# Kernel optimization log

Hardware: AMD Instinct MI355X
Metric: run time of the kernel (lower is better)

The kernel has to match this reference:

```python
import jax, jax.numpy as jnp
import numpy as np

NEG = -1e10  # the original uses -10000000000.0
B, T, L = 64, 512, 64
START, END = 0, L - 1


def setup_inputs() -> dict:
    key = jax.random.key(0)
    k_em, k_tr, k_len = jax.random.split(key, 3)
    emission_scores = jax.random.normal(k_em, (B, T, L), dtype=jnp.float32)
    # transition initialized as in __init__: randn with start column / end row masked
    transition = jax.random.normal(k_tr, (L, L), dtype=jnp.float32)
    transition = transition.at[:, START].set(NEG)
    transition = transition.at[END, :].set(NEG)
    sent_lens = jax.random.randint(k_len, (B,), T // 2, T + 1, dtype=jnp.int32)
    return {"emission_scores": emission_scores, "transition": transition,
            "sent_lens": sent_lens}


def reference(emission_scores, transition, sent_lens):
    # --- calculate_all_scores ---
    em = emission_scores.at[:, :, START].set(NEG).at[:, :, END].set(NEG)
    # scores[b,t,y_prev,y_t] = transition[y_prev,y_t] + emission[b,t,y_t]
    scores = transition[None, None, :, :] + em[:, :, None, :]  # [B,T,L,L]
    scores = scores.at[:, 1:, START, :].set(NEG)

    # --- forward_score: sequential DP via scan ---
    alpha0 = scores[:, 0, START, :]  # [B,L]

    def step(alpha_prev, s_t):  # s_t: [B,L,L]
        alpha_t = jax.nn.logsumexp(alpha_prev[:, :, None] + s_t, axis=1)
        return alpha_t, alpha_t

    _, alphas_rest = jax.lax.scan(step, alpha0, jnp.moveaxis(scores[:, 1:], 1, 0))
    alpha = jnp.concatenate([alpha0[:, None, :], jnp.moveaxis(alphas_rest, 0, 1)],
                            axis=1)  # [B,T,L]

    idx = (sent_lens - 1).astype(jnp.int32)[:, None, None]  # [B,1,1]
    last_alpha = jnp.take_along_axis(alpha, idx, axis=1)[:, 0, :]  # [B,L]
    last_alpha = last_alpha + transition[:, END][None, :]
    log_Z = jax.nn.logsumexp(last_alpha, axis=1)  # [B]
    return alpha, log_Z
```

## Files before the change

### kernel.cpp

```cpp
#include <hip/hip_runtime.h>

#define NEGV -10000000000.0f
constexpr int Bn = 64, Tn = 512, Ln = 64;
constexpr int CK = 32;
constexpr int NC = 16;
constexpr int QP = 64;

typedef float f32x16 __attribute__((ext_vector_type(16)));
typedef __bf16 bf16x8 __attribute__((ext_vector_type(8)));
typedef unsigned int u32;
typedef unsigned short u16;
typedef unsigned int u32x2 __attribute__((ext_vector_type(2)));

__device__ inline float waveMaxF(float v) {
#pragma unroll
    for (int off = 32; off > 0; off >>= 1)
        v = fmaxf(v, __shfl_xor(v, off, 64));
    return v;
}
__device__ inline u32 packbf(float a, float b) {
    u32 ua = __float_as_uint(a) + 0x8000u;
    u32 ub = __float_as_uint(b) + 0x8000u;
    return (ua >> 16) | (ub & 0xffff0000u);
}
__device__ inline u32 cvtpk(float a, float b) {
    u32 r;
    asm("v_cvt_pk_bf16_f32 %0, %1, %2" : "=v"(r) : "v"(a), "v"(b));
    return r;
}
__device__ inline void swap32(u32& x, u32& y) {
    u32x2 r = __builtin_amdgcn_permlane32_swap(x, y, false, false);
    x = r.x;
    y = r.y;
}
__device__ inline float lo16f(u32 d) { return __uint_as_float(d << 16); }
__device__ inline float hi16f(u32 d) { return __uint_as_float(d & 0xffff0000u); }

template <bool FIRST>
__device__ void chunk_scan(const float* __restrict__ emb,
                           float* __restrict__ outb, float* uLDS,
                           const float* Ecol, float entry, int t0, int j, int len,
                           float trSj, float* aLastOut, float* aFinalOut) {
    const bool edge = (j == 0) || (j == Ln - 1);
    float emq[4];
#pragma unroll
    for (int tt = 0; tt < 4; ++tt) {
        float v = emb[(t0 + tt) * Ln + j];
        emq[tt] = edge ? NEGV : v;
    }
    float aPrev, mPrev, u;
    int tauStart;
    if (FIRST) {
        float a0 = trSj + emq[0];
        outb[t0 * Ln + j] = a0;
        aPrev = a0;
        mPrev = __shfl(a0, 1, 64);
        u = __expf(a0 - mPrev);
        tauStart = 1;
    } else {
        aPrev = entry;
        mPrev = __shfl(entry, 1, 64);
        u = __expf(entry - mPrev);
        tauStart = 0;
    }
    float aLast = *aLastOut;
#pragma unroll 4
    for (int tau = tauStart; tau < CK; ++tau) {
        const int t = t0 + tau;
        uLDS[j] = u;
        const float em_t = emq[tau & 3];
        const int tp = tau + 4;
        if (tp < CK) {
            float v = emb[(t0 + tp) * Ln + j];
            emq[tp & 3] = edge ? NEGV : v;
        }
        float mNext = __shfl(aPrev, 1, 64);
        float cf = __expf(em_t + (mPrev - mNext));
        float acc0 = 0.f, acc1 = 0.f, acc2 = 0.f, acc3 = 0.f;
        const float4* u4 = reinterpret_cast<const float4*>(uLDS);
#pragma unroll
        for (int i4 = 0; i4 < 16; ++i4) {
            float4 uv = u4[i4];
            acc0 = fmaf(uv.x, Ecol[4 * i4 + 0], acc0);
            acc1 = fmaf(uv.y, Ecol[4 * i4 + 1], acc1);
            acc2 = fmaf(uv.z, Ecol[4 * i4 + 2], acc2);
            acc3 = fmaf(uv.w, Ecol[4 * i4 + 3], acc3);
        }
        float S = (acc0 + acc1) + (acc2 + acc3);
        float lg = __logf(S);
        lg = (S > 0.f) ? lg : NEGV;
        float a_t = em_t + (mPrev + lg);
        outb[t * Ln + j] = a_t;
        if (t == len - 1) aLast = a_t;
        u = S * cf;
        aPrev = a_t;
        mPrev = mNext;
    }
    *aLastOut = aLast;
    *aFinalOut = aPrev;
}

__global__ __launch_bounds__(128) void crf_passA(const float* __restrict__ em,
                                                 const float* __restrict__ tr,
                                                 float* __restrict__ out,
                                                 float* __restrict__ wsE,
                                                 float* __restrict__ wsS) {
    const int b = blockIdx.x & 63;
    const int cix = blockIdx.x >> 6;
    const int J = threadIdx.x >> 6;
    const int L = threadIdx.x & 63;
    __shared__ alignas(16) float gtab[CK * 64];
    __shared__ alignas(16) u16 Qlds[64 * QP];
    __shared__ alignas(16) float uLDS[64];
    __shared__ float sLDS[2];
    __shared__ float sigLDS[2];

    if (cix == 0) {
        if (J == 1) return;
        float Ecol[Ln];
#pragma unroll
        for (int i = 0; i < Ln; ++i) Ecol[i] = __expf(tr[i * Ln + L]);
        const float trSj = tr[L];
        const float* emb = em + (size_t)b * Tn * Ln;
        float* outb = out + (size_t)b * Tn * Ln;
        float dummyLast = 0.f, aFinal;
        chunk_scan<true>(emb, outb, uLDS, Ecol, 0.f, 0, L,  -1, trSj, &dummyLast, &aFinal);
        wsE[b * 1024 + 1 * 64 + L] = aFinal;
        return;
    }

    const int t0 = CK * cix;
    const int c31 = L & 31;
    const int h = L >> 5;

    {
        float orig[16], sv[16];
        const int tb = t0 + 16 * J;
#pragma unroll
        for (int r = 0; r < 16; ++r) {
            float v = em[((size_t)b * Tn + (tb + r)) * Ln + L];
            if (L == 0 || L == Ln - 1) v = NEGV;
            orig[r] = v;
            sv[r] = v;
        }
#pragma unroll
        for (int off = 32; off > 0; off >>= 1) {
#pragma unroll
            for (int r = 0; r < 16; ++r)
                sv[r] = fmaxf(sv[r], __shfl_xor(sv[r], off, 64));
        }
        float ssum = 0.f;
#pragma unroll
        for (int r = 0; r < 16; ++r) {
            gtab[(16 * J + r) * 64 + L] = __expf(orig[r] - sv[r]);
            ssum += sv[r];
        }
        if (L == 0) sLDS[J] = ssum;
    }
    __syncthreads();
    const float sSum = sLDS[0] + sLDS[1];

    uint4 Ap[2][4];
#pragma unroll
    for (int I = 0; I < 2; ++I)
#pragma unroll
        for (int kc = 0; kc < 4; ++kc) {
            float e[8];
#pragma unroll
            for (int q = 0; q < 8; ++q) {
                int k = 16 * kc + 8 * h + q;
                e[q] = __expf(tr[k * Ln + 32 * I + c31]);
            }
            Ap[I][kc] = make_uint4(packbf(e[0], e[1]), packbf(e[2], e[3]),
                                   packbf(e[4], e[5]), packbf(e[6], e[7]));
        }

    const int n = 32 * J + c31;
    uint4 Bp[4];
    {
        const float* trn = tr + n * Ln;
#pragma unroll
        for (int kc = 0; kc < 4; ++kc) {
            float v[8];
#pragma unroll
            for (int q = 0; q < 8; ++q) {
                const int k = 16 * kc + 8 * h + q;
                v[q] = __expf(trn[k]) * gtab[k];
            }
            Bp[kc] = make_uint4(cvtpk(v[0], v[1]), cvtpk(v[2], v[3]),
                                cvtpk(v[4], v[5]), cvtpk(v[6], v[7]));
        }
    }

    float sig_w = 0.f;
    float wm = 1.0f;
    const f32x16 Z = (f32x16)(0.0f);
    for (int tau = 1; tau < CK; ++tau) {
        f32x16 acc0 = Z, acc1 = Z;
#pragma unroll
        for (int kc = 0; kc < 4; ++kc) {
            acc0 = __builtin_amdgcn_mfma_f32_32x32x16_bf16(
                __builtin_bit_cast(bf16x8, Ap[0][kc]),
                __builtin_bit_cast(bf16x8, Bp[kc]), acc0, 0, 0, 0);
            acc1 = __builtin_amdgcn_mfma_f32_32x32x16_bf16(
                __builtin_bit_cast(bf16x8, Ap[1][kc]),
                __builtin_bit_cast(bf16x8, Bp[kc]), acc1, 0, 0, 0);
        }
        const bool doRescale = ((tau & 3) == 0);
        const bool doMeasure = ((tau & 3) == 2);
        float rr = 1.0f;
        if (doRescale) {
            rr = 1.0f / wm;
            sig_w += __logf(wm);
        }
        float lmax = 0.f;
        const float* gt = gtab + tau * 64;
#pragma unroll
        for (int I = 0; I < 2; ++I) {
            u32 pp[8];
#pragma unroll
            for (int rg = 0; rg < 4; ++rg) {
                const int k0 = 32 * I + 8 * rg + 4 * h;
                float4 G = *(const float4*)&gt[k0];
                float v0 = (I ? acc1 : acc0)[4 * rg + 0] * (G.x * rr);
                float v1 = (I ? acc1 : acc0)[4 * rg + 1] * (G.y * rr);
                float v2 = (I ? acc1 : acc0)[4 * rg + 2] * (G.z * rr);
                float v3 = (I ? acc1 : acc0)[4 * rg + 3] * (G.w * rr);
                if (doMeasure) lmax = fmaxf(lmax, fmaxf(fmaxf(v0, v1), fmaxf(v2, v3)));
                pp[2 * rg + 0] = cvtpk(v0, v1);
                pp[2 * rg + 1] = cvtpk(v2, v3);
            }
            swap32(pp[0], pp[2]);
            swap32(pp[1], pp[3]);
            swap32(pp[4], pp[6]);
            swap32(pp[5], pp[7]);
            Bp[2 * I + 0] = make_uint4(pp[0], pp[1], pp[2], pp[3]);
            Bp[2 * I + 1] = make_uint4(pp[4], pp[5], pp[6], pp[7]);
        }
        if (doMeasure) wm = waveMaxF(lmax);
    }

#pragma unroll
    for (int kc = 0; kc < 4; ++kc)
        *(uint4*)&Qlds[n * QP + 16 * kc + 8 * h] = Bp[kc];

    if (L == 0) sigLDS[J] = sSum + sig_w;
    __syncthreads();
    const float sg0 = sigLDS[0], sg1 = sigLDS[1];
    const float smax = fmaxf(sg0, sg1);
    const float fh = __expf((h ? sg1 : sg0) - smax);
    const int r = 32 * J + c31;
    float rv[32];
    float lmaxr = 0.f;
#pragma unroll
    for (int i = 0; i < 32; ++i) {
        float v = __uint_as_float(((u32)Qlds[(32 * h + i) * QP + r]) << 16) * fh;
        rv[i] = v;
        lmaxr = fmaxf(lmaxr, v);
    }
    float rmax = fmaxf(lmaxr, __shfl_xor(lmaxr, 32, 64));
    float inv = (rmax > 0.f) ? 1.0f / rmax : 0.f;
    float sj = (rmax > 0.f) ? smax + __logf(rmax) : 0.f;
    u32* og = (u32*)out + (size_t)b * (Tn * Ln) + (size_t)cix * (CK * Ln) + r * 32 + h * 16;
#pragma unroll
    for (int w8 = 0; w8 < 4; ++w8) {
        uint4 w;
        w.x = packbf(rv[8 * w8 + 0] * inv, rv[8 * w8 + 1] * inv);
        w.y = packbf(rv[8 * w8 + 2] * inv, rv[8 * w8 + 3] * inv);
        w.z = packbf(rv[8 * w8 + 4] * inv, rv[8 * w8 + 5] * inv);
        w.w = packbf(rv[8 * w8 + 6] * inv, rv[8 * w8 + 7] * inv);
        *(uint4*)(og + 4 * w8) = w;
    }
    if (h == 0) wsS[b * 1024 + cix * 64 + r] = sj;
}

__global__ __launch_bounds__(64) void crf_passB(const float* __restrict__ out,
                                                float* __restrict__ wsE,
                                                const float* __restrict__ wsS) {
    const int b = blockIdx.x;
    const int j = threadIdx.x;
    __shared__ alignas(16) float uL[64];
    const u32* Qbase = (const u32*)out + (size_t)b * (Tn * Ln);

    float e = wsE[b * 1024 + 1 * 64 + j];
    uint4 nxt[8];
    float signxt = wsS[b * 1024 + 1 * 64 + j];
#pragma unroll
    for (int r = 0; r < 8; ++r) nxt[r] = *(const uint4*)(Qbase + 1 * (CK * Ln) + j * 32 + 4 * r);

#pragma unroll
    for (int c = 1; c <= 14; ++c) {
        uint4 cur[8];
#pragma unroll
        for (int r = 0; r < 8; ++r) cur[r] = nxt[r];
        float sig = signxt;
        if (c < 14) {
#pragma unroll
            for (int r = 0; r < 8; ++r)
                nxt[r] = *(const uint4*)(Qbase + (size_t)(c + 1) * (CK * Ln) + j * 32 + 4 * r);
            signxt = wsS[b * 1024 + (c + 1) * 64 + j];
        }
        float m = __shfl(e, 1, 64);
        uL[j] = __expf(e - m);
        const float4* u4 = reinterpret_cast<const float4*>(uL);
        float S = 0.f;
#pragma unroll
        for (int i4 = 0; i4 < 16; ++i4) {
            float4 uv = u4[i4];
            u32 d0 = ((const u32*)cur)[2 * i4];
            u32 d1 = ((const u32*)cur)[2 * i4 + 1];
            S = fmaf(uv.x, lo16f(d0), S);
            S = fmaf(uv.y, hi16f(d0), S);
            S = fmaf(uv.z, lo16f(d1), S);
            S = fmaf(uv.w, hi16f(d1), S);
        }
        float a;
        if (S > 0.f) a = m + sig + __logf(S);
        else a = m + NEGV + ((j == 0) ? NEGV : 0.f);
        e = a;
        wsE[b * 1024 + (c + 1) * 64 + j] = e;
    }
}

__global__ __launch_bounds__(64) void crf_passC(const float* __restrict__ em,
                                                const float* __restrict__ tr,
                                                const int* __restrict__ lens,
                                                float* __restrict__ out,
                                                const float* __restrict__ wsE) {
    const int b = blockIdx.x & 63;
    const int cix = 1 + (blockIdx.x >> 6);
    const int j = threadIdx.x;
    __shared__ alignas(16) float uLDS[64];

    float Ecol[Ln];
#pragma unroll
    for (int i = 0; i < Ln; ++i) Ecol[i] = __expf(tr[i * Ln + j]);
    const float trEj = tr[j * Ln + (Ln - 1)];
    const int len = lens[b];
    const float* emb = em + (size_t)b * Tn * Ln;
    float* outb = out + (size_t)b * Tn * Ln;
    const float entry = wsE[b * 1024 + cix * 64 + j];

    float aLast = 0.f, aFinal;
    chunk_scan<false>(emb, outb, uLDS, Ecol, entry, CK * cix, j, len, 0.f, &aLast, &aFinal);

    if (((len - 1) >> 5) == cix) {
        float last = aLast + trEj;
        float m2 = last;
#pragma unroll
        for (int off = 32; off > 0; off >>= 1)
            m2 = fmaxf(m2, __shfl_xor(m2, off, 64));
        float e2 = __expf(last - m2);
#pragma unroll
        for (int off = 32; off > 0; off >>= 1)
            e2 += __shfl_xor(e2, off, 64);
        if (j == 0) out[(size_t)Bn * Tn * Ln + b] = m2 + __logf(e2);
    }
}

__global__ __launch_bounds__(64) void crf_fallback(const float* __restrict__ em,
                                                   const float* __restrict__ tr,
                                                   const int* __restrict__ lens,
                                                   float* __restrict__ out) {
    const int b = blockIdx.x;
    const int j = threadIdx.x;
    __shared__ alignas(16) float uLDS[Ln];
    float E[Ln];
#pragma unroll
    for (int i = 0; i < Ln; ++i) E[i] = __expf(tr[i * Ln + j]);
    const float trSj = tr[j];
    const float trEj = tr[j * Ln + (Ln - 1)];
    const int len = lens[b];
    const bool edge = (j == 0) || (j == Ln - 1);
    const float* emb = em + (size_t)b * Tn * Ln;
    float* outb = out + (size_t)b * Tn * Ln;
    float emq[4];
#pragma unroll
    for (int tt = 0; tt < 4; ++tt) {
        float v = emb[tt * Ln + j];
        emq[tt] = edge ? NEGV : v;
    }
    float a = trSj + emq[0];
    outb[j] = a;
    float aPrev = a, aLast = a;
    float mPrev = __shfl(a, 1, 64);
    float u = __expf(a - mPrev);
#pragma unroll 4
    for (int t = 1; t < Tn; ++t) {
        uLDS[j] = u;
        const float em_t = emq[t & 3];
        const int tp = t + 4;
        if (tp < Tn) {
            float v = emb[tp * Ln + j];
            emq[tp & 3] = edge ? NEGV : v;
        }
        float mNext = __shfl(aPrev, 1, 64);
        float cf = __expf(em_t + (mPrev - mNext));
        float acc0 = 0.f, acc1 = 0.f, acc2 = 0.f, acc3 = 0.f;
        const float4* u4 = reinterpret_cast<const float4*>(uLDS);
#pragma unroll
        for (int i4 = 0; i4 < 16; ++i4) {
            float4 uv = u4[i4];
            acc0 = fmaf(uv.x, E[4 * i4 + 0], acc0);
            acc1 = fmaf(uv.y, E[4 * i4 + 1], acc1);
            acc2 = fmaf(uv.z, E[4 * i4 + 2], acc2);
            acc3 = fmaf(uv.w, E[4 * i4 + 3], acc3);
        }
        float S = (acc0 + acc1) + (acc2 + acc3);
        float lg = __logf(S);
        lg = (S > 0.f) ? lg : NEGV;
        float a_t = em_t + (mPrev + lg);
        outb[t * Ln + j] = a_t;
        if (t == len - 1) aLast = a_t;
        u = S * cf;
        aPrev = a_t;
        mPrev = mNext;
    }
    float last = aLast + trEj;
    float m2 = last;
#pragma unroll
    for (int off = 32; off > 0; off >>= 1)
        m2 = fmaxf(m2, __shfl_xor(m2, off, 64));
    float e2 = __expf(last - m2);
#pragma unroll
    for (int off = 32; off > 0; off >>= 1)
        e2 += __shfl_xor(e2, off, 64);
    if (j == 0) out[(size_t)Bn * Tn * Ln + b] = m2 + __logf(e2);
}

extern "C" void kernel_launch(void* const* d_in, const int* in_sizes, int n_in,
                              void* d_out, int out_size, void* d_ws, size_t ws_size,
                              hipStream_t stream) {
    const float* em = (const float*)d_in[0];
    const float* tr = (const float*)d_in[1];
    const int* lens = (const int*)d_in[2];
    float* out = (float*)d_out;
    const size_t wsNeed = 2u * 64 * 16 * 64 * sizeof(float);
    if (ws_size >= wsNeed) {
        float* wsE = (float*)d_ws;
        float* wsS = wsE + 64 * 16 * 64;
        crf_passA<<<dim3(1024), dim3(128), 0, stream>>>(em, tr, out, wsE, wsS);
        crf_passB<<<dim3(64), dim3(64), 0, stream>>>(out, wsE, wsS);
        crf_passC<<<dim3(960), dim3(64), 0, stream>>>(em, tr, lens, out, wsE);
    } else {
        crf_fallback<<<dim3(Bn), dim3(64), 0, stream>>>(em, tr, lens, out);
    }
}
```

Before: 126.4 us.

## Split per-chunk transfer-matrix product into two half-chunk waves pairs and merge via MFMA

Pass A now uses four waves per block: one pair computes the forward product of the first half of the 32-step chunk, the other pair computes the second half (built from transposed transitions in reverse). The two half-chunk products are then combined with one extra MFMA matrix multiply through swizzled LDS. This halves the serial dependency chain of MFMA steps per chunk. In exchange it adds extra LDS traffic, barriers and a merge step, doubles the threads per block, and may change bf16 rounding behaviour.

```diff
diff --git a/kernel.cpp b/kernel.cpp
--- a/kernel.cpp
+++ b/kernel.cpp
@@ -35,6 +35,39 @@
 }
 __device__ inline float lo16f(u32 d) { return __uint_as_float(d << 16); }
 __device__ inline float hi16f(u32 d) { return __uint_as_float(d & 0xffff0000u); }
+
+__device__ inline void c2b(const f32x16& a0, const f32x16& a1, const float* gt,
+                           float rr, bool useG, bool doMeasure, float& lmax,
+                           uint4* Bp, int h) {
+#pragma unroll
+    for (int I = 0; I < 2; ++I) {
+        u32 pp[8];
+#pragma unroll
+        for (int rg = 0; rg < 4; ++rg) {
+            const int k0 = 32 * I + 8 * rg + 4 * h;
+            float gx, gy, gz, gw;
+            if (useG) {
+                float4 G = *(const float4*)&gt[k0];
+                gx = G.x * rr; gy = G.y * rr; gz = G.z * rr; gw = G.w * rr;
+            } else {
+                gx = gy = gz = gw = rr;
+            }
+            float v0 = (I ? a1 : a0)[4 * rg + 0] * gx;
+            float v1 = (I ? a1 : a0)[4 * rg + 1] * gy;
+            float v2 = (I ? a1 : a0)[4 * rg + 2] * gz;
+            float v3 = (I ? a1 : a0)[4 * rg + 3] * gw;
+            if (doMeasure) lmax = fmaxf(lmax, fmaxf(fmaxf(v0, v1), fmaxf(v2, v3)));
+            pp[2 * rg + 0] = cvtpk(v0, v1);
+            pp[2 * rg + 1] = cvtpk(v2, v3);
+        }
+        swap32(pp[0], pp[2]);
+        swap32(pp[1], pp[3]);
+        swap32(pp[4], pp[6]);
+        swap32(pp[5], pp[7]);
+        Bp[2 * I + 0] = make_uint4(pp[0], pp[1], pp[2], pp[3]);
+        Bp[2 * I + 1] = make_uint4(pp[4], pp[5], pp[6], pp[7]);
+    }
+}
 
 template <bool FIRST>
 __device__ void chunk_scan(const float* __restrict__ emb,
@@ -100,23 +133,25 @@
     *aFinalOut = aPrev;
 }
 
-__global__ __launch_bounds__(128) void crf_passA(const float* __restrict__ em,
-                                                 const float* __restrict__ tr,
-                                                 float* __restrict__ out,
-                                                 float* __restrict__ wsE,
-                                                 float* __restrict__ wsS) {
+__global__ __launch_bounds__(256, 4) void crf_passA(const float* __restrict__ em,
+                                                    const float* __restrict__ tr,
+                                                    float* __restrict__ out,
+                                                    float* __restrict__ wsE,
+                                                    float* __restrict__ wsS) {
     const int b = blockIdx.x & 63;
     const int cix = blockIdx.x >> 6;
     const int J = threadIdx.x >> 6;
     const int L = threadIdx.x & 63;
+    const int J2 = J & 1;
+    const int pair = J >> 1;
     __shared__ alignas(16) float gtab[CK * 64];
     __shared__ alignas(16) u16 Qlds[64 * QP];
     __shared__ alignas(16) float uLDS[64];
-    __shared__ float sLDS[2];
-    __shared__ float sigLDS[2];
+    __shared__ float sLDS[4];
+    __shared__ float sigLDS[4];
 
     if (cix == 0) {
-        if (J == 1) return;
+        if (J != 0) return;
         float Ecol[Ln];
 #pragma unroll
         for (int i = 0; i < Ln; ++i) Ecol[i] = __expf(tr[i * Ln + L]);
@@ -134,10 +169,10 @@
     const int h = L >> 5;
 
     {
-        float orig[16], sv[16];
-        const int tb = t0 + 16 * J;
-#pragma unroll
-        for (int r = 0; r < 16; ++r) {
+        float orig[8], sv[8];
+        const int tb = t0 + 8 * J;
+#pragma unroll
+        for (int r = 0; r < 8; ++r) {
             float v = em[((size_t)b * Tn + (tb + r)) * Ln + L];
             if (L == 0 || L == Ln - 1) v = NEGV;
             orig[r] = v;
@@ -146,19 +181,19 @@
 #pragma unroll
         for (int off = 32; off > 0; off >>= 1) {
 #pragma unroll
-            for (int r = 0; r < 16; ++r)
+            for (int r = 0; r < 8; ++r)
                 sv[r] = fmaxf(sv[r], __shfl_xor(sv[r], off, 64));
         }
         float ssum = 0.f;
 #pragma unroll
-        for (int r = 0; r < 16; ++r) {
-            gtab[(16 * J + r) * 64 + L] = __expf(orig[r] - sv[r]);
+        for (int r = 0; r < 8; ++r) {
+            gtab[(8 * J + r) * 64 + L] = __expf(orig[r] - sv[r]);
             ssum += sv[r];
         }
         if (L == 0) sLDS[J] = ssum;
     }
     __syncthreads();
-    const float sSum = sLDS[0] + sLDS[1];
+    const float sSeg = sLDS[2 * pair] + sLDS[2 * pair + 1];
 
     uint4 Ap[2][4];
 #pragma unroll
@@ -169,15 +204,16 @@
 #pragma unroll
             for (int q = 0; q < 8; ++q) {
                 int k = 16 * kc + 8 * h + q;
-                e[q] = __expf(tr[k * Ln + 32 * I + c31]);
+                int m = 32 * I + c31;
+                e[q] = __expf(pair ? tr[m * Ln + k] : tr[k * Ln + m]);
             }
             Ap[I][kc] = make_uint4(packbf(e[0], e[1]), packbf(e[2], e[3]),
                                    packbf(e[4], e[5]), packbf(e[6], e[7]));
         }
 
-    const int n = 32 * J + c31;
+    const int n = 32 * J2 + c31;
     uint4 Bp[4];
-    {
+    if (pair == 0) {
         const float* trn = tr + n * Ln;
 #pragma unroll
         for (int kc = 0; kc < 4; ++kc) {
@@ -190,12 +226,25 @@
             Bp[kc] = make_uint4(cvtpk(v[0], v[1]), cvtpk(v[2], v[3]),
                                 cvtpk(v[4], v[5]), cvtpk(v[6], v[7]));
         }
+    } else {
+        const float gn = gtab[31 * 64 + n];
+#pragma unroll
+        for (int kc = 0; kc < 4; ++kc) {
+            float v[8];
+#pragma unroll
+            for (int q = 0; q < 8; ++q) {
+                const int k = 16 * kc + 8 * h + q;
+                v[q] = __expf(tr[k * Ln + n]) * gtab[30 * 64 + k] * gn;
+            }
+            Bp[kc] = make_uint4(cvtpk(v[0], v[1]), cvtpk(v[2], v[3]),
+                                cvtpk(v[4], v[5]), cvtpk(v[6], v[7]));
+        }
     }
 
     float sig_w = 0.f;
     float wm = 1.0f;
     const f32x16 Z = (f32x16)(0.0f);
-    for (int tau = 1; tau < CK; ++tau) {
+    for (int lt = 1; lt <= 15; ++lt) {
         f32x16 acc0 = Z, acc1 = Z;
 #pragma unroll
         for (int kc = 0; kc < 4; ++kc) {
@@ -206,46 +255,77 @@
                 __builtin_bit_cast(bf16x8, Ap[1][kc]),
                 __builtin_bit_cast(bf16x8, Bp[kc]), acc1, 0, 0, 0);
         }
-        const bool doRescale = ((tau & 3) == 0);
-        const bool doMeasure = ((tau & 3) == 2);
+        const bool doRescale = ((lt & 3) == 0);
+        const bool doMeasure = ((lt & 3) == 2);
         float rr = 1.0f;
         if (doRescale) {
             rr = 1.0f / wm;
             sig_w += __logf(wm);
         }
+        const int grow = pair ? (30 - lt) : lt;
+        const bool useG = !(pair && lt == 15);
         float lmax = 0.f;
-        const float* gt = gtab + tau * 64;
-#pragma unroll
-        for (int I = 0; I < 2; ++I) {
-            u32 pp[8];
-#pragma unroll
-            for (int rg = 0; rg < 4; ++rg) {
-                const int k0 = 32 * I + 8 * rg + 4 * h;
-                float4 G = *(const float4*)&gt[k0];
-                float v0 = (I ? acc1 : acc0)[4 * rg + 0] * (G.x * rr);
-                float v1 = (I ? acc1 : acc0)[4 * rg + 1] * (G.y * rr);
-                float v2 = (I ? acc1 : acc0)[4 * rg + 2] * (G.z * rr);
-                float v3 = (I ? acc1 : acc0)[4 * rg + 3] * (G.w * rr);
-                if (doMeasure) lmax = fmaxf(lmax, fmaxf(fmaxf(v0, v1), fmaxf(v2, v3)));
-                pp[2 * rg + 0] = cvtpk(v0, v1);
-                pp[2 * rg + 1] = cvtpk(v2, v3);
+        c2b(acc0, acc1, gtab + grow * 64, rr, useG, doMeasure, lmax, Bp, h);
+        if (doMeasure) wm = waveMaxF(lmax);
+    }
+
+    if (L == 0) sigLDS[J] = sSeg + sig_w;
+    __syncthreads();
+    const float smax1 = fmaxf(sigLDS[2], sigLDS[3]);
+
+    if (pair == 1) {
+        const float fh1 = __expf(sigLDS[J] - smax1);
+        const u32 swz = (u32)(n & 7) << 4;
+        char* base = (char*)Qlds;
+#pragma unroll
+        for (int kc = 0; kc < 4; ++kc) {
+            uint4 w = Bp[kc];
+            float s0 = lo16f(w.x) * fh1, s1 = hi16f(w.x) * fh1;
+            float s2 = lo16f(w.y) * fh1, s3 = hi16f(w.y) * fh1;
+            float s4 = lo16f(w.z) * fh1, s5 = hi16f(w.z) * fh1;
+            float s6 = lo16f(w.w) * fh1, s7 = hi16f(w.w) * fh1;
+            uint4 o = make_uint4(cvtpk(s0, s1), cvtpk(s2, s3), cvtpk(s4, s5), cvtpk(s6, s7));
+            *(uint4*)(base + (((u32)(n * 128 + 32 * kc + 16 * h)) ^ swz)) = o;
+        }
+    }
+    __syncthreads();
+
+    uint4 BpZ[4];
+    if (pair == 0) {
+        uint4 Ah[2][4];
+        const char* cbase = (const char*)Qlds;
+#pragma unroll
+        for (int I = 0; I < 2; ++I)
+#pragma unroll
+            for (int kc = 0; kc < 4; ++kc) {
+                const int m = 32 * I + c31;
+                Ah[I][kc] = *(const uint4*)(cbase +
+                    (((u32)(m * 128 + 32 * kc + 16 * h)) ^ ((u32)(m & 7) << 4)));
             }
-            swap32(pp[0], pp[2]);
-            swap32(pp[1], pp[3]);
-            swap32(pp[4], pp[6]);
-            swap32(pp[5], pp[7]);
-            Bp[2 * I + 0] = make_uint4(pp[0], pp[1], pp[2], pp[3]);
-            Bp[2 * I + 1] = make_uint4(pp[4], pp[5], pp[6], pp[7]);
-        }
-        if (doMeasure) wm = waveMaxF(lmax);
-    }
-
-#pragma unroll
-    for (int kc = 0; kc < 4; ++kc)
-        *(uint4*)&Qlds[n * QP + 16 * kc + 8 * h] = Bp[kc];
-
-    if (L == 0) sigLDS[J] = sSum + sig_w;
+        f32x16 acc0 = Z, acc1 = Z;
+#pragma unroll
+        for (int kc = 0; kc < 4; ++kc) {
+            acc0 = __builtin_amdgcn_mfma_f32_32x32x16_bf16(
+                __builtin_bit_cast(bf16x8, Ah[0][kc]),
+                __builtin_bit_cast(bf16x8, Bp[kc]), acc0, 0, 0, 0);
+            acc1 = __builtin_amdgcn_mfma_f32_32x32x16_bf16(
+                __builtin_bit_cast(bf16x8, Ah[1][kc]),
+                __builtin_bit_cast(bf16x8, Bp[kc]), acc1, 0, 0, 0);
+        }
+        float dummy = 0.f;
+        c2b(acc0, acc1, nullptr, 1.0f, false, false, dummy, BpZ, h);
+    }
     __syncthreads();
+
+    if (pair == 0) {
+#pragma unroll
+        for (int kc = 0; kc < 4; ++kc)
+            *(uint4*)&Qlds[n * QP + 16 * kc + 8 * h] = BpZ[kc];
+        if (L == 0) sigLDS[J] += smax1;
+    }
+    __syncthreads();
+    if (pair == 1) return;
+
     const float sg0 = sigLDS[0], sg1 = sigLDS[1];
     const float smax = fmaxf(sg0, sg1);
     const float fh = __expf((h ? sg1 : sg0) - smax);
@@ -439,7 +519,7 @@
     if (ws_size >= wsNeed) {
         float* wsE = (float*)d_ws;
         float* wsS = wsE + 64 * 16 * 64;
-        crf_passA<<<dim3(1024), dim3(128), 0, stream>>>(em, tr, out, wsE, wsS);
+        crf_passA<<<dim3(1024), dim3(256), 0, stream>>>(em, tr, out, wsE, wsS);
         crf_passB<<<dim3(64), dim3(64), 0, stream>>>(out, wsE, wsS);
         crf_passC<<<dim3(960), dim3(64), 0, stream>>>(em, tr, lens, out, wsE);
     } else {
```

New measurement: 138.0 us. +9.2%, slower.

## Halve chunk length, precompute exp(transition) tables, stage chunk matrices in workspace

Applied to the files above, without the earlier changes.

Chunk length drops from 32 to 16 steps, doubling the chunks per sequence so the per-chunk matrix scan and the final per-chunk rescan (passC) are shorter and more parallel. The serial combine pass (passB) now runs 30 steps instead of 14. A new pre-kernel computes exp(transition) once, in fp32 and as a transposed bf16 table, so passA and passC load it instead of recomputing exp per block. Chunk transfer matrices now go to a dedicated workspace buffer instead of being parked in the output, at the cost of an extra launch and more workspace traffic.

```diff
diff --git a/kernel.cpp b/kernel.cpp
--- a/kernel.cpp
+++ b/kernel.cpp
@@ -2,9 +2,10 @@
 
 #define NEGV -10000000000.0f
 constexpr int Bn = 64, Tn = 512, Ln = 64;
-constexpr int CK = 32;
-constexpr int NC = 16;
+constexpr int CK = 16;
+constexpr int NC = 32;
 constexpr int QP = 64;
+constexpr int WS = 2048;
 
 typedef float f32x16 __attribute__((ext_vector_type(16)));
 typedef __bf16 bf16x8 __attribute__((ext_vector_type(8)));
@@ -35,6 +36,42 @@
 }
 __device__ inline float lo16f(u32 d) { return __uint_as_float(d << 16); }
 __device__ inline float hi16f(u32 d) { return __uint_as_float(d & 0xffff0000u); }
+
+__device__ inline void c2b(const f32x16& a0, const f32x16& a1, const float* gt,
+                           float rr, bool doMeasure, float& lmax, uint4* Bp, int h) {
+#pragma unroll
+    for (int I = 0; I < 2; ++I) {
+        u32 pp[8];
+#pragma unroll
+        for (int rg = 0; rg < 4; ++rg) {
+            const int k0 = 32 * I + 8 * rg + 4 * h;
+            float4 G = *(const float4*)&gt[k0];
+            float v0 = (I ? a1 : a0)[4 * rg + 0] * (G.x * rr);
+            float v1 = (I ? a1 : a0)[4 * rg + 1] * (G.y * rr);
+            float v2 = (I ? a1 : a0)[4 * rg + 2] * (G.z * rr);
+            float v3 = (I ? a1 : a0)[4 * rg + 3] * (G.w * rr);
+            if (doMeasure) lmax = fmaxf(lmax, fmaxf(fmaxf(v0, v1), fmaxf(v2, v3)));
+            pp[2 * rg + 0] = cvtpk(v0, v1);
+            pp[2 * rg + 1] = cvtpk(v2, v3);
+        }
+        swap32(pp[0], pp[2]);
+        swap32(pp[1], pp[3]);
+        swap32(pp[4], pp[6]);
+        swap32(pp[5], pp[7]);
+        Bp[2 * I + 0] = make_uint4(pp[0], pp[1], pp[2], pp[3]);
+        Bp[2 * I + 1] = make_uint4(pp[4], pp[5], pp[6], pp[7]);
+    }
+}
+
+__global__ __launch_bounds__(64) void crf_pre(const float* __restrict__ tr,
+                                              float* __restrict__ tblR,
+                                              u16* __restrict__ tblT) {
+    const int id = blockIdx.x * 64 + threadIdx.x;
+    tblR[id] = __expf(tr[id]);
+    const int m = id >> 6, k = id & 63;
+    float ev = __expf(tr[k * Ln + m]);
+    tblT[id] = (u16)cvtpk(ev, ev);
+}
 
 template <bool FIRST>
 __device__ void chunk_scan(const float* __restrict__ emb,
@@ -102,9 +139,12 @@
 
 __global__ __launch_bounds__(128) void crf_passA(const float* __restrict__ em,
                                                  const float* __restrict__ tr,
+                                                 const float* __restrict__ tblR,
+                                                 const u16* __restrict__ tblT,
                                                  float* __restrict__ out,
                                                  float* __restrict__ wsE,
-                                                 float* __restrict__ wsS) {
+                                                 float* __restrict__ wsS,
+                                                 u32* __restrict__ wsT) {
     const int b = blockIdx.x & 63;
     const int cix = blockIdx.x >> 6;
     const int J = threadIdx.x >> 6;
@@ -119,13 +159,13 @@
         if (J == 1) return;
         float Ecol[Ln];
 #pragma unroll
-        for (int i = 0; i < Ln; ++i) Ecol[i] = __expf(tr[i * Ln + L]);
+        for (int i = 0; i < Ln; ++i) Ecol[i] = tblR[i * Ln + L];
         const float trSj = tr[L];
         const float* emb = em + (size_t)b * Tn * Ln;
         float* outb = out + (size_t)b * Tn * Ln;
         float dummyLast = 0.f, aFinal;
         chunk_scan<true>(emb, outb, uLDS, Ecol, 0.f, 0, L,  -1, trSj, &dummyLast, &aFinal);
-        wsE[b * 1024 + 1 * 64 + L] = aFinal;
+        wsE[b * WS + 1 * 64 + L] = aFinal;
         return;
     }
 
@@ -134,10 +174,10 @@
     const int h = L >> 5;
 
     {
-        float orig[16], sv[16];
-        const int tb = t0 + 16 * J;
-#pragma unroll
-        for (int r = 0; r < 16; ++r) {
+        float orig[8], sv[8];
+        const int tb = t0 + 8 * J;
+#pragma unroll
+        for (int r = 0; r < 8; ++r) {
             float v = em[((size_t)b * Tn + (tb + r)) * Ln + L];
             if (L == 0 || L == Ln - 1) v = NEGV;
             orig[r] = v;
@@ -146,13 +186,13 @@
 #pragma unroll
         for (int off = 32; off > 0; off >>= 1) {
 #pragma unroll
-            for (int r = 0; r < 16; ++r)
+            for (int r = 0; r < 8; ++r)
                 sv[r] = fmaxf(sv[r], __shfl_xor(sv[r], off, 64));
         }
         float ssum = 0.f;
 #pragma unroll
-        for (int r = 0; r < 16; ++r) {
-            gtab[(16 * J + r) * 64 + L] = __expf(orig[r] - sv[r]);
+        for (int r = 0; r < 8; ++r) {
+            gtab[(8 * J + r) * 64 + L] = __expf(orig[r] - sv[r]);
             ssum += sv[r];
         }
         if (L == 0) sLDS[J] = ssum;
@@ -161,34 +201,30 @@
     const float sSum = sLDS[0] + sLDS[1];
 
     uint4 Ap[2][4];
-#pragma unroll
-    for (int I = 0; I < 2; ++I)
-#pragma unroll
-        for (int kc = 0; kc < 4; ++kc) {
-            float e[8];
-#pragma unroll
-            for (int q = 0; q < 8; ++q) {
-                int k = 16 * kc + 8 * h + q;
-                e[q] = __expf(tr[k * Ln + 32 * I + c31]);
-            }
-            Ap[I][kc] = make_uint4(packbf(e[0], e[1]), packbf(e[2], e[3]),
-                                   packbf(e[4], e[5]), packbf(e[6], e[7]));
-        }
+    {
+        const uint4* Af = (const uint4*)tblT;
+#pragma unroll
+        for (int I = 0; I < 2; ++I)
+#pragma unroll
+            for (int kc = 0; kc < 4; ++kc)
+                Ap[I][kc] = Af[(32 * I + c31) * 8 + 2 * kc + h];
+    }
 
     const int n = 32 * J + c31;
     uint4 Bp[4];
     {
-        const float* trn = tr + n * Ln;
+        const float* trn = tblR + n * Ln;
 #pragma unroll
         for (int kc = 0; kc < 4; ++kc) {
-            float v[8];
-#pragma unroll
-            for (int q = 0; q < 8; ++q) {
-                const int k = 16 * kc + 8 * h + q;
-                v[q] = __expf(trn[k]) * gtab[k];
-            }
-            Bp[kc] = make_uint4(cvtpk(v[0], v[1]), cvtpk(v[2], v[3]),
-                                cvtpk(v[4], v[5]), cvtpk(v[6], v[7]));
+            const int k0 = 16 * kc + 8 * h;
+            float4 e0 = *(const float4*)&trn[k0];
+            float4 e1 = *(const float4*)&trn[k0 + 4];
+            float4 g0 = *(const float4*)&gtab[k0];
+            float4 g1 = *(const float4*)&gtab[k0 + 4];
+            Bp[kc] = make_uint4(cvtpk(e0.x * g0.x, e0.y * g0.y),
+                                cvtpk(e0.z * g0.z, e0.w * g0.w),
+                                cvtpk(e1.x * g1.x, e1.y * g1.y),
+                                cvtpk(e1.z * g1.z, e1.w * g1.w));
         }
     }
 
@@ -214,29 +250,7 @@
             sig_w += __logf(wm);
         }
         float lmax = 0.f;
-        const float* gt = gtab + tau * 64;
-#pragma unroll
-        for (int I = 0; I < 2; ++I) {
-            u32 pp[8];
-#pragma unroll
-            for (int rg = 0; rg < 4; ++rg) {
-                const int k0 = 32 * I + 8 * rg + 4 * h;
-                float4 G = *(const float4*)&gt[k0];
-                float v0 = (I ? acc1 : acc0)[4 * rg + 0] * (G.x * rr);
-                float v1 = (I ? acc1 : acc0)[4 * rg + 1] * (G.y * rr);
-                float v2 = (I ? acc1 : acc0)[4 * rg + 2] * (G.z * rr);
-                float v3 = (I ? acc1 : acc0)[4 * rg + 3] * (G.w * rr);
-                if (doMeasure) lmax = fmaxf(lmax, fmaxf(fmaxf(v0, v1), fmaxf(v2, v3)));
-                pp[2 * rg + 0] = cvtpk(v0, v1);
-                pp[2 * rg + 1] = cvtpk(v2, v3);
-            }
-            swap32(pp[0], pp[2]);
-            swap32(pp[1], pp[3]);
-            swap32(pp[4], pp[6]);
-            swap32(pp[5], pp[7]);
-            Bp[2 * I + 0] = make_uint4(pp[0], pp[1], pp[2], pp[3]);
-            Bp[2 * I + 1] = make_uint4(pp[4], pp[5], pp[6], pp[7]);
-        }
+        c2b(acc0, acc1, gtab + tau * 64, rr, doMeasure, lmax, Bp, h);
         if (doMeasure) wm = waveMaxF(lmax);
     }
 
@@ -261,7 +275,7 @@
     float rmax = fmaxf(lmaxr, __shfl_xor(lmaxr, 32, 64));
     float inv = (rmax > 0.f) ? 1.0f / rmax : 0.f;
     float sj = (rmax > 0.f) ? smax + __logf(rmax) : 0.f;
-    u32* og = (u32*)out + (size_t)b * (Tn * Ln) + (size_t)cix * (CK * Ln) + r * 32 + h * 16;
+    u32* og = wsT + (size_t)(b * NC + cix) * 2048 + r * 32 + h * 16;
 #pragma unroll
     for (int w8 = 0; w8 < 4; ++w8) {
         uint4 w;
@@ -271,34 +285,33 @@
         w.w = packbf(rv[8 * w8 + 6] * inv, rv[8 * w8 + 7] * inv);
         *(uint4*)(og + 4 * w8) = w;
     }
-    if (h == 0) wsS[b * 1024 + cix * 64 + r] = sj;
-}
-
-__global__ __launch_bounds__(64) void crf_passB(const float* __restrict__ out,
+    if (h == 0) wsS[b * WS + cix * 64 + r] = sj;
+}
+
+__global__ __launch_bounds__(64) void crf_passB(const u32* __restrict__ wsT,
                                                 float* __restrict__ wsE,
                                                 const float* __restrict__ wsS) {
     const int b = blockIdx.x;
     const int j = threadIdx.x;
     __shared__ alignas(16) float uL[64];
-    const u32* Qbase = (const u32*)out + (size_t)b * (Tn * Ln);
-
-    float e = wsE[b * 1024 + 1 * 64 + j];
+    const u32* Qbase = wsT + (size_t)b * NC * 2048;
+
+    float e = wsE[b * WS + 1 * 64 + j];
     uint4 nxt[8];
-    float signxt = wsS[b * 1024 + 1 * 64 + j];
-#pragma unroll
-    for (int r = 0; r < 8; ++r) nxt[r] = *(const uint4*)(Qbase + 1 * (CK * Ln) + j * 32 + 4 * r);
-
-#pragma unroll
-    for (int c = 1; c <= 14; ++c) {
+    float signxt = wsS[b * WS + 1 * 64 + j];
+#pragma unroll
+    for (int r = 0; r < 8; ++r) nxt[r] = *(const uint4*)(Qbase + 1 * 2048 + j * 32 + 4 * r);
+
+    for (int c = 1; c <= NC - 2; ++c) {
         uint4 cur[8];
 #pragma unroll
         for (int r = 0; r < 8; ++r) cur[r] = nxt[r];
         float sig = signxt;
-        if (c < 14) {
+        if (c < NC - 2) {
 #pragma unroll
             for (int r = 0; r < 8; ++r)
-                nxt[r] = *(const uint4*)(Qbase + (size_t)(c + 1) * (CK * Ln) + j * 32 + 4 * r);
-            signxt = wsS[b * 1024 + (c + 1) * 64 + j];
+                nxt[r] = *(const uint4*)(Qbase + (size_t)(c + 1) * 2048 + j * 32 + 4 * r);
+            signxt = wsS[b * WS + (c + 1) * 64 + j];
         }
         float m = __shfl(e, 1, 64);
         uL[j] = __expf(e - m);
@@ -318,11 +331,12 @@
         if (S > 0.f) a = m + sig + __logf(S);
         else a = m + NEGV + ((j == 0) ? NEGV : 0.f);
         e = a;
-        wsE[b * 1024 + (c + 1) * 64 + j] = e;
+        wsE[b * WS + (c + 1) * 64 + j] = e;
     }
 }
 
 __global__ __launch_bounds__(64) void crf_passC(const float* __restrict__ em,
+                                                const float* __restrict__ tblR,
                                                 const float* __restrict__ tr,
                                                 const int* __restrict__ lens,
                                                 float* __restrict__ out,
@@ -334,17 +348,17 @@
 
     float Ecol[Ln];
 #pragma unroll
-    for (int i = 0; i < Ln; ++i) Ecol[i] = __expf(tr[i * Ln + j]);
+    for (int i = 0; i < Ln; ++i) Ecol[i] = tblR[i * Ln + j];
     const float trEj = tr[j * Ln + (Ln - 1)];
     const int len = lens[b];
     const float* emb = em + (size_t)b * Tn * Ln;
     float* outb = out + (size_t)b * Tn * Ln;
-    const float entry = wsE[b * 1024 + cix * 64 + j];
+    const float entry = wsE[b * WS + cix * 64 + j];
 
     float aLast = 0.f, aFinal;
     chunk_scan<false>(emb, outb, uLDS, Ecol, entry, CK * cix, j, len, 0.f, &aLast, &aFinal);
 
-    if (((len - 1) >> 5) == cix) {
+    if (((len - 1) >> 4) == cix) {
         float last = aLast + trEj;
         float m2 = last;
 #pragma unroll
@@ -435,13 +449,17 @@
     const float* tr = (const float*)d_in[1];
     const int* lens = (const int*)d_in[2];
     float* out = (float*)d_out;
-    const size_t wsNeed = 2u * 64 * 16 * 64 * sizeof(float);
+    const size_t wsNeed = (6144 + 2 * 64 * WS) * sizeof(float) + (size_t)64 * NC * 2048 * sizeof(u32);
     if (ws_size >= wsNeed) {
-        float* wsE = (float*)d_ws;
-        float* wsS = wsE + 64 * 16 * 64;
-        crf_passA<<<dim3(1024), dim3(128), 0, stream>>>(em, tr, out, wsE, wsS);
-        crf_passB<<<dim3(64), dim3(64), 0, stream>>>(out, wsE, wsS);
-        crf_passC<<<dim3(960), dim3(64), 0, stream>>>(em, tr, lens, out, wsE);
+        float* tblR = (float*)d_ws;
+        u16* tblT = (u16*)(tblR + 4096);
+        float* wsE = tblR + 6144;
+        float* wsS = wsE + 64 * WS;
+        u32* wsT = (u32*)(wsS + 64 * WS);
+        crf_pre<<<dim3(64), dim3(64), 0, stream>>>(tr, tblR, tblT);
+        crf_passA<<<dim3(64 * NC), dim3(128), 0, stream>>>(em, tr, tblR, tblT, out, wsE, wsS, wsT);
+        crf_passB<<<dim3(64), dim3(64), 0, stream>>>(wsT, wsE, wsS);
+        crf_passC<<<dim3(64 * (NC - 1)), dim3(64), 0, stream>>>(em, tblR, tr, lens, out, wsE);
     } else {
         crf_fallback<<<dim3(Bn), dim3(64), 0, stream>>>(em, tr, lens, out);
     }
```

Measured after the change: 137.3 us. 8.7% more time.
